# Performance work log

Hardware: AMD Instinct MI355X
Metric: run time of the kernel (lower is better)

## Reference

```python
import jax, jax.numpy as jnp
import numpy as np

MAX_WAVELENGTH = 10000.0
NUM_HEADS = 15
NUM_KV_HEADS = 5
HEAD_DIM = 64


def apply_rope(x, positions):
    """RoPE: x [B, L, H, D], positions [B, L] (int)."""
    d_half = x.shape[-1] // 2
    x = x.astype(jnp.float32)
    freq_exponents = (2.0 / x.shape[-1]) * jnp.arange(d_half, dtype=jnp.float32)
    timescale = MAX_WAVELENGTH ** freq_exponents  # [d_half]
    radians = positions[..., None].astype(jnp.float32) / timescale  # [B, L, d_half]
    radians = radians[..., None, :]  # [B, L, 1, d_half]
    sin, cos = jnp.sin(radians), jnp.cos(radians)
    x1, x2 = x[..., :d_half], x[..., d_half:]
    return jnp.concatenate([x1 * cos - x2 * sin, x2 * cos + x1 * sin], axis=-1)


def setup_inputs() -> dict:
    key = jax.random.key(0)
    k1, k2, k3, k4 = jax.random.split(key, 4)
    B, L = 2, 2048
    query_states = jax.random.normal(k1, (B, L, NUM_HEADS, HEAD_DIM), dtype=jnp.float32)
    key_states = jax.random.normal(k2, (B, L, NUM_KV_HEADS, HEAD_DIM), dtype=jnp.float32)
    value_states = jax.random.normal(k3, (B, L, NUM_KV_HEADS, HEAD_DIM), dtype=jnp.float32)
    positions = jnp.sort(jax.random.randint(k4, (B, L), 0, L, dtype=jnp.int32), axis=-1)
    # Causal (prefix-LM) boolean mask [B, L, L]
    attention_mask = jnp.broadcast_to(jnp.tril(jnp.ones((L, L), dtype=bool)), (B, L, L))
    return {
        "query_states": query_states,
        "key_states": key_states,
        "value_states": value_states,
        "positions": positions,
        "attention_mask": attention_mask,
    }


def reference(query_states, key_states, value_states, positions, attention_mask):
    B, L = query_states.shape[0], query_states.shape[1]
    groups = NUM_HEADS // NUM_KV_HEADS  # 3

    # RoPE on Q and K (eager, per original module)
    q = apply_rope(query_states, positions)  # [B, L, 15, 64] fp32
    k = apply_rope(key_states, positions)    # [B, L, 5, 64]  fp32

    # GQA expansion: [B, L, Kv, D] -> [B, L, Kv*groups, D]
    k = jnp.repeat(k, groups, axis=2)
    v = jnp.repeat(value_states, groups, axis=2).astype(jnp.float32)

    # Scores in fp32: [B, H, Lq, Lk]
    scores = jnp.einsum("bqhd,bkhd->bhqk", q, k) * (HEAD_DIM ** -0.5)
    big_neg = jnp.finfo(jnp.float32).min
    scores = jnp.where(attention_mask[:, None, :, :], scores, big_neg)
    probs = jax.nn.softmax(scores, axis=-1)

    out = jnp.einsum("bhqk,bkhd->bqhd", probs, v)  # [B, L, H, D]
    return out.reshape(B, L, NUM_HEADS * HEAD_DIM)  # [B, L, 960]
```

## Files before the change

### kernel.cpp

```cpp
#include <hip/hip_runtime.h>
#include <math.h>

#define NB 2
#define NL 2048
#define NHQ 15
#define NKV 5
#define HD 64
#define NT 32
#define GRP 3
#define PST 72

typedef __attribute__((ext_vector_type(8))) short short8;
typedef __attribute__((ext_vector_type(4))) float floatx4;

#define ROPE_C 0.28782313662425575f
#define QSCALE 0.18033688011116016f

__device__ __forceinline__ ushort f2bf(float x) {
    unsigned u = __builtin_bit_cast(unsigned, x);
    u = (u + 0x7FFFu + ((u >> 16) & 1u)) >> 16;
    return (ushort)u;
}
__device__ __forceinline__ unsigned pk2(float a, float b) {
    unsigned ua = __builtin_bit_cast(unsigned, a) + 0x8000u;
    unsigned ub = __builtin_bit_cast(unsigned, b) + 0x8000u;
    return __builtin_amdgcn_perm(ub, ua, 0x07060302u);
}
__device__ __forceinline__ void async16(ushort* lds, const ushort* g) {
    __builtin_amdgcn_global_load_lds(
        (const __attribute__((address_space(1))) unsigned int*)g,
        (__attribute__((address_space(3))) unsigned int*)lds, 16, 0, 0);
}

union U8  { short8 v; ushort u[8]; };
union F8  { float4 f4[2]; float f[8]; };

__global__ __launch_bounds__(256)
void prep_kv(const float* __restrict__ K, const float* __restrict__ V,
             const int* __restrict__ pos, ushort* __restrict__ Kr,
             ushort* __restrict__ Vr) {
    __shared__ float Vs[64][65];
    const int bid = blockIdx.x, t = threadIdx.x;
    if (bid < NB * NKV * NT) {
        int b = bid / (NKV * NT), rem = bid % (NKV * NT);
        int h = rem / NT, k0 = (rem % NT) * 64;
        int j = t >> 2, c0 = t & 3;
        int row = k0 + j;
        const float* src = K + ((size_t)((b * NL + row) * NKV + h)) * HD;
        int db = c0 * 8;
        F8 x1, x2;
        x1.f4[0] = *(const float4*)&src[db];
        x1.f4[1] = *(const float4*)&src[db + 4];
        x2.f4[0] = *(const float4*)&src[db + 32];
        x2.f4[1] = *(const float4*)&src[db + 36];
        float ps = (float)pos[b * NL + row];
        U8 lo, hi;
#pragma unroll
        for (int i = 0; i < 8; ++i) {
            float inv = __expf((float)(db + i) * -ROPE_C);
            float sn, cs; __sincosf(ps * inv, &sn, &cs);
            lo.u[i] = f2bf(x1.f[i] * cs - x2.f[i] * sn);
            hi.u[i] = f2bf(x2.f[i] * cs + x1.f[i] * sn);
        }
        ushort* dst = Kr + (size_t)bid * 4096;
        *(short8*)&dst[(j * 8 + (c0 ^ (j & 7))) * 8]       = lo.v;
        *(short8*)&dst[(j * 8 + ((c0 + 4) ^ (j & 7))) * 8] = hi.v;
    } else {
        int vb = bid - NB * NKV * NT;
        int b = vb / (NKV * NT), rem = vb % (NKV * NT);
        int h = rem / NT, k0 = (rem % NT) * 64;
#pragma unroll
        for (int it = 0; it < 4; ++it) {
            int e = t + it * 256;
            int j = e >> 4, d4 = (e & 15) * 4;
            *(float4*)&Vs[j][d4] =
                *(const float4*)&V[((size_t)((b * NL + k0 + j) * NKV + h)) * HD + d4];
        }
        __syncthreads();
        ushort* dst = Vr + (size_t)vb * 4096;
#pragma unroll
        for (int it = 0; it < 2; ++it) {
            int o = t + it * 256;
            int d = o >> 3, c = o & 7, j0 = c * 8;
            U8 r;
#pragma unroll
            for (int k = 0; k < 8; ++k) r.u[k] = f2bf(Vs[j0 + k][d]);
            *(short8*)&dst[(d * 8 + (c ^ (d & 7))) * 8] = r.v;
        }
    }
}

__global__ __launch_bounds__(256, 1)
void attn_flash(const float* __restrict__ Q, const ushort* __restrict__ Kr,
                const ushort* __restrict__ Vr, const int* __restrict__ pos,
                float* __restrict__ out) {
    __shared__ __align__(16) ushort Kb[2][4096];
    __shared__ __align__(16) ushort Vb[2][4096];
    __shared__ __align__(16) ushort Pb[4][2][16 * PST];

    const int t = threadIdx.x;
    const int w = t >> 6, lane = t & 63;
    const int l16 = lane & 15, quad = lane >> 4;

    const int bid  = blockIdx.x;
    const int work = (bid & 7) * 30 + (bid >> 3);
    const int pi = work & 7;
    int rem = work >> 3;
    const int hg = rem % 3; rem /= 3;
    const int kvh = rem % 5;
    const int b = rem / 5;
    const int h = kvh * GRP + hg;

    const ushort* Kt0 = Kr + (size_t)((b * NKV + kvh) * NT) * 4096;
    const ushort* Vt0 = Vr + (size_t)((b * NKV + kvh) * NT) * 4096;
    const int swz8[2] = { ((quad)     ^ (l16 & 7)) * 8,
                          ((quad + 4) ^ (l16 & 7)) * 8 };
    const int so = w * 1024;

    for (int ph = 0; ph < 2; ++ph) {
        const int g   = ph ? (15 - pi) : pi;
        const int qi  = 4 * g + w;
        const int ntb = 2 * g + 2;
        const int ntw = (qi >> 1) + 1;
        const int r0  = qi * 32;

        async16(&Kb[0][so],       Kt0 + so + lane * 8);
        async16(&Kb[0][so + 512], Kt0 + so + 512 + lane * 8);
        async16(&Vb[0][so],       Vt0 + so + lane * 8);
        async16(&Vb[0][so + 512], Vt0 + so + 512 + lane * 8);

        short8 Qa[2][2];
#pragma unroll
        for (int rf = 0; rf < 2; ++rf) {
            int row = r0 + rf * 16 + l16;
            const float* src = Q + ((size_t)((b * NL + row) * NHQ + h)) * HD;
            int db = quad * 8;
            F8 x1, x2;
            x1.f4[0] = *(const float4*)&src[db];
            x1.f4[1] = *(const float4*)&src[db + 4];
            x2.f4[0] = *(const float4*)&src[db + 32];
            x2.f4[1] = *(const float4*)&src[db + 36];
            float ps = (float)pos[b * NL + row];
            union { short8 v; unsigned u[4]; } lo, hi;
#pragma unroll
            for (int i = 0; i < 8; i += 2) {
                float inv0 = __expf((float)(db + i) * -ROPE_C);
                float inv1 = __expf((float)(db + i + 1) * -ROPE_C);
                float sn0, cs0, sn1, cs1;
                __sincosf(ps * inv0, &sn0, &cs0);
                __sincosf(ps * inv1, &sn1, &cs1);
                float lo0 = (x1.f[i] * cs0 - x2.f[i] * sn0) * QSCALE;
                float lo1 = (x1.f[i + 1] * cs1 - x2.f[i + 1] * sn1) * QSCALE;
                float hi0 = (x2.f[i] * cs0 + x1.f[i] * sn0) * QSCALE;
                float hi1 = (x2.f[i + 1] * cs1 + x1.f[i + 1] * sn1) * QSCALE;
                lo.u[i >> 1] = pk2(lo0, lo1);
                hi.u[i >> 1] = pk2(hi0, hi1);
            }
            Qa[rf][0] = lo.v;
            Qa[rf][1] = hi.v;
        }

        floatx4 O[2][4];
        float lsum[2] = {0.f, 0.f};
#pragma unroll
        for (int rf = 0; rf < 2; ++rf)
#pragma unroll
            for (int d = 0; d < 4; ++d) O[rf][d] = (floatx4){0.f, 0.f, 0.f, 0.f};

        __syncthreads();

        int cur = 0;
        for (int kb = 0; kb < ntb; ++kb) {
            if (kb + 1 < ntb) {
                const ushort* Kt = Kt0 + (size_t)(kb + 1) * 4096;
                const ushort* Vt = Vt0 + (size_t)(kb + 1) * 4096;
                const int nx = cur ^ 1;
                async16(&Kb[nx][so],       Kt + so + lane * 8);
                async16(&Kb[nx][so + 512], Kt + so + 512 + lane * 8);
                async16(&Vb[nx][so],       Vt + so + lane * 8);
                async16(&Vb[nx][so + 512], Vt + so + 512 + lane * 8);
            }

            if (kb < ntw) {
                floatx4 S[2][4];
#pragma unroll
                for (int rf = 0; rf < 2; ++rf)
#pragma unroll
                    for (int c = 0; c < 4; ++c) S[rf][c] = (floatx4){0.f, 0.f, 0.f, 0.f};
#pragma unroll
                for (int s = 0; s < 2; ++s)
#pragma unroll
                    for (int c = 0; c < 4; ++c) {
                        short8 kfv = *(const short8*)&Kb[cur][(c * 16 + l16) * 64 + swz8[s]];
                        S[0][c] = __builtin_amdgcn_mfma_f32_16x16x32_bf16(kfv, Qa[0][s], S[0][c], 0, 0, 0);
                        S[1][c] = __builtin_amdgcn_mfma_f32_16x16x32_bf16(kfv, Qa[1][s], S[1][c], 0, 0, 0);
                    }

                if (kb == ntw - 1) {
#pragma unroll
                    for (int rf = 0; rf < 2; ++rf) {
                        int qrow = r0 + rf * 16 + l16;
                        float acc = 0.f;
#pragma unroll
                        for (int c = 0; c < 4; ++c) {
                            float pv[4];
#pragma unroll
                            for (int r = 0; r < 4; ++r) {
                                int key = kb * 64 + c * 16 + quad * 4 + r;
                                float sv = S[rf][c][r];
                                if (key > qrow) sv = -1e30f;
                                pv[r] = exp2f(sv);
                                acc += pv[r];
                            }
                            *(uint2*)&Pb[w][rf][l16 * PST + c * 16 + quad * 4] =
                                make_uint2(pk2(pv[0], pv[1]), pk2(pv[2], pv[3]));
                        }
                        lsum[rf] += acc;
                    }
                } else {
#pragma unroll
                    for (int rf = 0; rf < 2; ++rf) {
                        float acc = 0.f;
#pragma unroll
                        for (int c = 0; c < 4; ++c) {
                            float pv[4];
#pragma unroll
                            for (int r = 0; r < 4; ++r) {
                                pv[r] = exp2f(S[rf][c][r]);
                                acc += pv[r];
                            }
                            *(uint2*)&Pb[w][rf][l16 * PST + c * 16 + quad * 4] =
                                make_uint2(pk2(pv[0], pv[1]), pk2(pv[2], pv[3]));
                        }
                        lsum[rf] += acc;
                    }
                }

#pragma unroll
                for (int s = 0; s < 2; ++s) {
                    short8 pf0 = *(const short8*)&Pb[w][0][l16 * PST + s * 32 + quad * 8];
                    short8 pf1 = *(const short8*)&Pb[w][1][l16 * PST + s * 32 + quad * 8];
#pragma unroll
                    for (int d = 0; d < 4; ++d) {
                        short8 vfv = *(const short8*)&Vb[cur][(d * 16 + l16) * 64 + swz8[s]];
                        O[0][d] = __builtin_amdgcn_mfma_f32_16x16x32_bf16(vfv, pf0, O[0][d], 0, 0, 0);
                        O[1][d] = __builtin_amdgcn_mfma_f32_16x16x32_bf16(vfv, pf1, O[1][d], 0, 0, 0);
                    }
                }
            }

            __syncthreads();
            cur ^= 1;
        }

#pragma unroll
        for (int rf = 0; rf < 2; ++rf) {
            float ls = lsum[rf];
            ls += __shfl_xor(ls, 16, 64);
            ls += __shfl_xor(ls, 32, 64);
            float rinv = 1.0f / ls;
            int qrow = r0 + rf * 16 + l16;
            float* op = out + (size_t)(b * NL + qrow) * (NHQ * HD) + h * HD;
#pragma unroll
            for (int d = 0; d < 4; ++d) {
                float4 o = make_float4(O[rf][d][0] * rinv, O[rf][d][1] * rinv,
                                       O[rf][d][2] * rinv, O[rf][d][3] * rinv);
                *(float4*)&op[d * 16 + quad * 4] = o;
            }
        }
    }
}

extern "C" void kernel_launch(void* const* d_in, const int* in_sizes, int n_in,
                              void* d_out, int out_size, void* d_ws, size_t ws_size,
                              hipStream_t stream) {
    const float* Q   = (const float*)d_in[0];
    const float* K   = (const float*)d_in[1];
    const float* V   = (const float*)d_in[2];
    const int*   pos = (const int*)d_in[3];
    ushort* Kr = (ushort*)d_ws;
    ushort* Vr = Kr + (size_t)NB * NKV * NT * 4096;
    float*  out = (float*)d_out;

    prep_kv<<<2 * NB * NKV * NT, 256, 0, stream>>>(K, V, pos, Kr, Vr);
    attn_flash<<<NB * NHQ * 8, 256, 0, stream>>>(Q, Kr, Vr, pos, out);
}
```

Measured before the change: 150.8 us.

## Load K/V tiles straight into registers in MFMA fragment layout, drop LDS staging

The prep kernel now writes K and V in a per-lane MFMA fragment order, so each wave loads its operands directly from global memory into registers with a software-prefetched double buffer. This removes the shared K/V LDS buffers, the async LDS copies and the per-tile block barriers. Each wave now walks only its own causal range independently. Work is redistributed across 480 blocks, with four balanced query tiles per block (k, 31-k, 32+k, 63-k), and launch bounds are raised to two blocks per CU. In exchange, every wave re-reads K/V from global/L2 instead of sharing one LDS copy, and register pressure rises from holding the current and next tiles.

Result: faster. 139.2 us (-7.7%).

```diff
diff --git a/kernel.cpp b/kernel.cpp
--- a/kernel.cpp
+++ b/kernel.cpp
@@ -25,11 +25,6 @@
     unsigned ua = __builtin_bit_cast(unsigned, a) + 0x8000u;
     unsigned ub = __builtin_bit_cast(unsigned, b) + 0x8000u;
     return __builtin_amdgcn_perm(ub, ua, 0x07060302u);
-}
-__device__ __forceinline__ void async16(ushort* lds, const ushort* g) {
-    __builtin_amdgcn_global_load_lds(
-        (const __attribute__((address_space(1))) unsigned int*)g,
-        (__attribute__((address_space(3))) unsigned int*)lds, 16, 0, 0);
 }
 
 union U8  { short8 v; ushort u[8]; };
@@ -63,8 +58,8 @@
             hi.u[i] = f2bf(x2.f[i] * cs + x1.f[i] * sn);
         }
         ushort* dst = Kr + (size_t)bid * 4096;
-        *(short8*)&dst[(j * 8 + (c0 ^ (j & 7))) * 8]       = lo.v;
-        *(short8*)&dst[(j * 8 + ((c0 + 4) ^ (j & 7))) * 8] = hi.v;
+        *(short8*)&dst[(((j >> 4)) * 64 + c0 * 16 + (j & 15)) * 8]     = lo.v;
+        *(short8*)&dst[((4 + (j >> 4)) * 64 + c0 * 16 + (j & 15)) * 8] = hi.v;
     } else {
         int vb = bid - NB * NKV * NT;
         int b = vb / (NKV * NT), rem = vb % (NKV * NT);
@@ -85,17 +80,15 @@
             U8 r;
 #pragma unroll
             for (int k = 0; k < 8; ++k) r.u[k] = f2bf(Vs[j0 + k][d]);
-            *(short8*)&dst[(d * 8 + (c ^ (d & 7))) * 8] = r.v;
-        }
-    }
-}
-
-__global__ __launch_bounds__(256, 1)
+            *(short8*)&dst[(((c >> 2) * 4 + (d >> 4)) * 64 + (c & 3) * 16 + (d & 15)) * 8] = r.v;
+        }
+    }
+}
+
+__global__ __launch_bounds__(256, 2)
 void attn_flash(const float* __restrict__ Q, const ushort* __restrict__ Kr,
                 const ushort* __restrict__ Vr, const int* __restrict__ pos,
                 float* __restrict__ out) {
-    __shared__ __align__(16) ushort Kb[2][4096];
-    __shared__ __align__(16) ushort Vb[2][4096];
     __shared__ __align__(16) ushort Pb[4][2][16 * PST];
 
     const int t = threadIdx.x;
@@ -103,170 +96,161 @@
     const int l16 = lane & 15, quad = lane >> 4;
 
     const int bid  = blockIdx.x;
-    const int work = (bid & 7) * 30 + (bid >> 3);
-    const int pi = work & 7;
-    int rem = work >> 3;
-    const int hg = rem % 3; rem /= 3;
-    const int kvh = rem % 5;
-    const int b = rem / 5;
-    const int h = kvh * GRP + hg;
+    const int work = (bid & 7) * 60 + (bid >> 3);
+    const int bh = work >> 4;
+    const int k  = work & 15;
+    const int b = bh / NHQ, h = bh % NHQ;
+    const int kvh = h / GRP;
+    const int qi = (w == 0) ? k : (w == 1) ? (31 - k) : (w == 2) ? (32 + k) : (63 - k);
+    const int ntw = (qi >> 1) + 1;
+    const int r0  = qi * 32;
 
     const ushort* Kt0 = Kr + (size_t)((b * NKV + kvh) * NT) * 4096;
     const ushort* Vt0 = Vr + (size_t)((b * NKV + kvh) * NT) * 4096;
-    const int swz8[2] = { ((quad)     ^ (l16 & 7)) * 8,
-                          ((quad + 4) ^ (l16 & 7)) * 8 };
-    const int so = w * 1024;
-
-    for (int ph = 0; ph < 2; ++ph) {
-        const int g   = ph ? (15 - pi) : pi;
-        const int qi  = 4 * g + w;
-        const int ntb = 2 * g + 2;
-        const int ntw = (qi >> 1) + 1;
-        const int r0  = qi * 32;
-
-        async16(&Kb[0][so],       Kt0 + so + lane * 8);
-        async16(&Kb[0][so + 512], Kt0 + so + 512 + lane * 8);
-        async16(&Vb[0][so],       Vt0 + so + lane * 8);
-        async16(&Vb[0][so + 512], Vt0 + so + 512 + lane * 8);
-
-        short8 Qa[2][2];
-#pragma unroll
-        for (int rf = 0; rf < 2; ++rf) {
-            int row = r0 + rf * 16 + l16;
-            const float* src = Q + ((size_t)((b * NL + row) * NHQ + h)) * HD;
-            int db = quad * 8;
-            F8 x1, x2;
-            x1.f4[0] = *(const float4*)&src[db];
-            x1.f4[1] = *(const float4*)&src[db + 4];
-            x2.f4[0] = *(const float4*)&src[db + 32];
-            x2.f4[1] = *(const float4*)&src[db + 36];
-            float ps = (float)pos[b * NL + row];
-            union { short8 v; unsigned u[4]; } lo, hi;
-#pragma unroll
-            for (int i = 0; i < 8; i += 2) {
-                float inv0 = __expf((float)(db + i) * -ROPE_C);
-                float inv1 = __expf((float)(db + i + 1) * -ROPE_C);
-                float sn0, cs0, sn1, cs1;
-                __sincosf(ps * inv0, &sn0, &cs0);
-                __sincosf(ps * inv1, &sn1, &cs1);
-                float lo0 = (x1.f[i] * cs0 - x2.f[i] * sn0) * QSCALE;
-                float lo1 = (x1.f[i + 1] * cs1 - x2.f[i + 1] * sn1) * QSCALE;
-                float hi0 = (x2.f[i] * cs0 + x1.f[i] * sn0) * QSCALE;
-                float hi1 = (x2.f[i + 1] * cs1 + x1.f[i + 1] * sn1) * QSCALE;
-                lo.u[i >> 1] = pk2(lo0, lo1);
-                hi.u[i >> 1] = pk2(hi0, hi1);
-            }
-            Qa[rf][0] = lo.v;
-            Qa[rf][1] = hi.v;
-        }
-
-        floatx4 O[2][4];
-        float lsum[2] = {0.f, 0.f};
+
+    short8 Qa[2][2];
+#pragma unroll
+    for (int rf = 0; rf < 2; ++rf) {
+        int row = r0 + rf * 16 + l16;
+        const float* src = Q + ((size_t)((b * NL + row) * NHQ + h)) * HD;
+        int db = quad * 8;
+        F8 x1, x2;
+        x1.f4[0] = *(const float4*)&src[db];
+        x1.f4[1] = *(const float4*)&src[db + 4];
+        x2.f4[0] = *(const float4*)&src[db + 32];
+        x2.f4[1] = *(const float4*)&src[db + 36];
+        float ps = (float)pos[b * NL + row];
+        union { short8 v; unsigned u[4]; } lo, hi;
+#pragma unroll
+        for (int i = 0; i < 8; i += 2) {
+            float inv0 = __expf((float)(db + i) * -ROPE_C);
+            float inv1 = __expf((float)(db + i + 1) * -ROPE_C);
+            float sn0, cs0, sn1, cs1;
+            __sincosf(ps * inv0, &sn0, &cs0);
+            __sincosf(ps * inv1, &sn1, &cs1);
+            float lo0 = (x1.f[i] * cs0 - x2.f[i] * sn0) * QSCALE;
+            float lo1 = (x1.f[i + 1] * cs1 - x2.f[i + 1] * sn1) * QSCALE;
+            float hi0 = (x2.f[i] * cs0 + x1.f[i] * sn0) * QSCALE;
+            float hi1 = (x2.f[i + 1] * cs1 + x1.f[i + 1] * sn1) * QSCALE;
+            lo.u[i >> 1] = pk2(lo0, lo1);
+            hi.u[i >> 1] = pk2(hi0, hi1);
+        }
+        Qa[rf][0] = lo.v;
+        Qa[rf][1] = hi.v;
+    }
+
+    floatx4 O[2][4];
+    float lsum[2] = {0.f, 0.f};
+#pragma unroll
+    for (int rf = 0; rf < 2; ++rf)
+#pragma unroll
+        for (int d = 0; d < 4; ++d) O[rf][d] = (floatx4){0.f, 0.f, 0.f, 0.f};
+
+    short8 kc[8], vc[8];
+#pragma unroll
+    for (int i = 0; i < 8; ++i) {
+        kc[i] = *(const short8*)&Kt0[((size_t)i * 64 + lane) * 8];
+        vc[i] = *(const short8*)&Vt0[((size_t)i * 64 + lane) * 8];
+    }
+
+    for (int kb = 0; kb < ntw; ++kb) {
+        short8 kn[8], vn[8];
+        const bool pf = (kb + 1 < ntw);
+        if (pf) {
+            const ushort* Kt = Kt0 + (size_t)(kb + 1) * 4096;
+            const ushort* Vt = Vt0 + (size_t)(kb + 1) * 4096;
+#pragma unroll
+            for (int i = 0; i < 8; ++i) {
+                kn[i] = *(const short8*)&Kt[((size_t)i * 64 + lane) * 8];
+                vn[i] = *(const short8*)&Vt[((size_t)i * 64 + lane) * 8];
+            }
+        }
+
+        floatx4 S[2][4];
 #pragma unroll
         for (int rf = 0; rf < 2; ++rf)
 #pragma unroll
-            for (int d = 0; d < 4; ++d) O[rf][d] = (floatx4){0.f, 0.f, 0.f, 0.f};
-
-        __syncthreads();
-
-        int cur = 0;
-        for (int kb = 0; kb < ntb; ++kb) {
-            if (kb + 1 < ntb) {
-                const ushort* Kt = Kt0 + (size_t)(kb + 1) * 4096;
-                const ushort* Vt = Vt0 + (size_t)(kb + 1) * 4096;
-                const int nx = cur ^ 1;
-                async16(&Kb[nx][so],       Kt + so + lane * 8);
-                async16(&Kb[nx][so + 512], Kt + so + 512 + lane * 8);
-                async16(&Vb[nx][so],       Vt + so + lane * 8);
-                async16(&Vb[nx][so + 512], Vt + so + 512 + lane * 8);
-            }
-
-            if (kb < ntw) {
-                floatx4 S[2][4];
-#pragma unroll
-                for (int rf = 0; rf < 2; ++rf)
-#pragma unroll
-                    for (int c = 0; c < 4; ++c) S[rf][c] = (floatx4){0.f, 0.f, 0.f, 0.f};
-#pragma unroll
-                for (int s = 0; s < 2; ++s)
-#pragma unroll
-                    for (int c = 0; c < 4; ++c) {
-                        short8 kfv = *(const short8*)&Kb[cur][(c * 16 + l16) * 64 + swz8[s]];
-                        S[0][c] = __builtin_amdgcn_mfma_f32_16x16x32_bf16(kfv, Qa[0][s], S[0][c], 0, 0, 0);
-                        S[1][c] = __builtin_amdgcn_mfma_f32_16x16x32_bf16(kfv, Qa[1][s], S[1][c], 0, 0, 0);
+            for (int c = 0; c < 4; ++c) S[rf][c] = (floatx4){0.f, 0.f, 0.f, 0.f};
+#pragma unroll
+        for (int s = 0; s < 2; ++s)
+#pragma unroll
+            for (int c = 0; c < 4; ++c) {
+                short8 kfv = kc[s * 4 + c];
+                S[0][c] = __builtin_amdgcn_mfma_f32_16x16x32_bf16(kfv, Qa[0][s], S[0][c], 0, 0, 0);
+                S[1][c] = __builtin_amdgcn_mfma_f32_16x16x32_bf16(kfv, Qa[1][s], S[1][c], 0, 0, 0);
+            }
+
+        if (kb == ntw - 1) {
+#pragma unroll
+            for (int rf = 0; rf < 2; ++rf) {
+                int qrow = r0 + rf * 16 + l16;
+                float acc = 0.f;
+#pragma unroll
+                for (int c = 0; c < 4; ++c) {
+                    float pv[4];
+#pragma unroll
+                    for (int r = 0; r < 4; ++r) {
+                        int key = kb * 64 + c * 16 + quad * 4 + r;
+                        float sv = S[rf][c][r];
+                        if (key > qrow) sv = -1e30f;
+                        pv[r] = exp2f(sv);
+                        acc += pv[r];
                     }
-
-                if (kb == ntw - 1) {
-#pragma unroll
-                    for (int rf = 0; rf < 2; ++rf) {
-                        int qrow = r0 + rf * 16 + l16;
-                        float acc = 0.f;
-#pragma unroll
-                        for (int c = 0; c < 4; ++c) {
-                            float pv[4];
-#pragma unroll
-                            for (int r = 0; r < 4; ++r) {
-                                int key = kb * 64 + c * 16 + quad * 4 + r;
-                                float sv = S[rf][c][r];
-                                if (key > qrow) sv = -1e30f;
-                                pv[r] = exp2f(sv);
-                                acc += pv[r];
-                            }
-                            *(uint2*)&Pb[w][rf][l16 * PST + c * 16 + quad * 4] =
-                                make_uint2(pk2(pv[0], pv[1]), pk2(pv[2], pv[3]));
-                        }
-                        lsum[rf] += acc;
+                    *(uint2*)&Pb[w][rf][l16 * PST + c * 16 + quad * 4] =
+                        make_uint2(pk2(pv[0], pv[1]), pk2(pv[2], pv[3]));
+                }
+                lsum[rf] += acc;
+            }
+        } else {
+#pragma unroll
+            for (int rf = 0; rf < 2; ++rf) {
+                float acc = 0.f;
+#pragma unroll
+                for (int c = 0; c < 4; ++c) {
+                    float pv[4];
+#pragma unroll
+                    for (int r = 0; r < 4; ++r) {
+                        pv[r] = exp2f(S[rf][c][r]);
+                        acc += pv[r];
                     }
-                } else {
-#pragma unroll
-                    for (int rf = 0; rf < 2; ++rf) {
-                        float acc = 0.f;
-#pragma unroll
-                        for (int c = 0; c < 4; ++c) {
-                            float pv[4];
-#pragma unroll
-                            for (int r = 0; r < 4; ++r) {
-                                pv[r] = exp2f(S[rf][c][r]);
-                                acc += pv[r];
-                            }
-                            *(uint2*)&Pb[w][rf][l16 * PST + c * 16 + quad * 4] =
-                                make_uint2(pk2(pv[0], pv[1]), pk2(pv[2], pv[3]));
-                        }
-                        lsum[rf] += acc;
-                    }
+                    *(uint2*)&Pb[w][rf][l16 * PST + c * 16 + quad * 4] =
+                        make_uint2(pk2(pv[0], pv[1]), pk2(pv[2], pv[3]));
                 }
-
-#pragma unroll
-                for (int s = 0; s < 2; ++s) {
-                    short8 pf0 = *(const short8*)&Pb[w][0][l16 * PST + s * 32 + quad * 8];
-                    short8 pf1 = *(const short8*)&Pb[w][1][l16 * PST + s * 32 + quad * 8];
-#pragma unroll
-                    for (int d = 0; d < 4; ++d) {
-                        short8 vfv = *(const short8*)&Vb[cur][(d * 16 + l16) * 64 + swz8[s]];
-                        O[0][d] = __builtin_amdgcn_mfma_f32_16x16x32_bf16(vfv, pf0, O[0][d], 0, 0, 0);
-                        O[1][d] = __builtin_amdgcn_mfma_f32_16x16x32_bf16(vfv, pf1, O[1][d], 0, 0, 0);
-                    }
-                }
-            }
-
-            __syncthreads();
-            cur ^= 1;
-        }
-
-#pragma unroll
-        for (int rf = 0; rf < 2; ++rf) {
-            float ls = lsum[rf];
-            ls += __shfl_xor(ls, 16, 64);
-            ls += __shfl_xor(ls, 32, 64);
-            float rinv = 1.0f / ls;
-            int qrow = r0 + rf * 16 + l16;
-            float* op = out + (size_t)(b * NL + qrow) * (NHQ * HD) + h * HD;
+                lsum[rf] += acc;
+            }
+        }
+
+#pragma unroll
+        for (int s = 0; s < 2; ++s) {
+            short8 pf0 = *(const short8*)&Pb[w][0][l16 * PST + s * 32 + quad * 8];
+            short8 pf1 = *(const short8*)&Pb[w][1][l16 * PST + s * 32 + quad * 8];
 #pragma unroll
             for (int d = 0; d < 4; ++d) {
-                float4 o = make_float4(O[rf][d][0] * rinv, O[rf][d][1] * rinv,
-                                       O[rf][d][2] * rinv, O[rf][d][3] * rinv);
-                *(float4*)&op[d * 16 + quad * 4] = o;
-            }
+                short8 vfv = vc[s * 4 + d];
+                O[0][d] = __builtin_amdgcn_mfma_f32_16x16x32_bf16(vfv, pf0, O[0][d], 0, 0, 0);
+                O[1][d] = __builtin_amdgcn_mfma_f32_16x16x32_bf16(vfv, pf1, O[1][d], 0, 0, 0);
+            }
+        }
+
+        if (pf) {
+#pragma unroll
+            for (int i = 0; i < 8; ++i) { kc[i] = kn[i]; vc[i] = vn[i]; }
+        }
+    }
+
+#pragma unroll
+    for (int rf = 0; rf < 2; ++rf) {
+        float ls = lsum[rf];
+        ls += __shfl_xor(ls, 16, 64);
+        ls += __shfl_xor(ls, 32, 64);
+        float rinv = 1.0f / ls;
+        int qrow = r0 + rf * 16 + l16;
+        float* op = out + (size_t)(b * NL + qrow) * (NHQ * HD) + h * HD;
+#pragma unroll
+        for (int d = 0; d < 4; ++d) {
+            float4 o = make_float4(O[rf][d][0] * rinv, O[rf][d][1] * rinv,
+                                   O[rf][d][2] * rinv, O[rf][d][3] * rinv);
+            *(float4*)&op[d * 16 + quad * 4] = o;
         }
     }
 }
@@ -283,5 +267,5 @@
     float*  out = (float*)d_out;
 
     prep_kv<<<2 * NB * NKV * NT, 256, 0, stream>>>(K, V, pos, Kr, Vr);
-    attn_flash<<<NB * NHQ * 8, 256, 0, stream>>>(Q, Kr, Vr, pos, out);
-}
+    attn_flash<<<NB * NHQ * 16, 256, 0, stream>>>(Q, Kr, Vr, pos, out);
+}
```
